# Performance work log

Measured on AMD Instinct MI355X. Metric: run time of the kernel, lower is better.

The kernel has to match this reference:

```python
import jax, jax.numpy as jnp
import numpy as np

N_T, D_MODEL, RANK, BATCH = 64, 1024, 8, 4096
THRESHOLD = 0.0  # jumprelu threshold (forward default)


def setup_inputs() -> dict:
    key = jax.random.key(0)
    k_x, k_v, k_u, k_e = jax.random.split(key, 4)
    scale = (1.0 / (D_MODEL * RANK)) ** 0.25
    x = jax.random.normal(k_x, (BATCH, D_MODEL), dtype=jnp.float32)
    V = jax.random.normal(k_v, (N_T, RANK, D_MODEL), dtype=jnp.float32) * scale
    U = jax.random.normal(k_u, (N_T, D_MODEL, RANK), dtype=jnp.float32) * scale
    encoder = jax.random.normal(k_e, (N_T, D_MODEL), dtype=jnp.float32)
    encoder = encoder / jnp.linalg.norm(encoder, axis=1, keepdims=True)
    bias = -jnp.ones((N_T,), dtype=jnp.float32)  # init_constant(bias, -1.0)
    return {"x": x, "V": V, "U": U, "encoder": encoder, "bias": bias}


def jumprelu(x, threshold=THRESHOLD):
    # forward: hard threshold x * 1[x > threshold]
    return x * (x > threshold).astype(x.dtype)


def reference(x, V, U, encoder, bias):
    # pre_acts: (batch, n)
    pre_acts = x @ encoder.T - bias
    gate = jumprelu(pre_acts)  # activation_fn='jumprelu', threshold=0.0
    # Vx: (n, batch, rank)
    Vx = jnp.einsum('nrd,bd->nbr', V, x)
    # UVx: (n, batch, d) -- the large intermediate a fused kernel would avoid
    UVx = jnp.einsum('ndr,nbr->nbd', U, Vx)
    # gated sum over transforms: (batch, d)
    output = jnp.einsum('nbd,bn->bd', UVx, gate)
    u_norms = jnp.linalg.norm(U.reshape(U.shape[0], -1), axis=1)
    v_norms = jnp.linalg.norm(V.reshape(V.shape[0], -1), axis=1)
    frobenius_norms = u_norms * v_norms / (D_MODEL * RANK) ** 0.5
    return output, gate, frobenius_norms
```

## Files before the change

kernel.cpp:

```cpp
#include <hip/hip_runtime.h>
#include <math.h>

#define BATCHN 4096
#define DMODEL 1024
#define NT 64
#define RANK 8
#define K2 512

typedef __attribute__((ext_vector_type(8))) short bf16x8;
typedef __attribute__((ext_vector_type(4))) float f32x4;

__device__ __forceinline__ void async16(void* lds, const void* g) {
    __builtin_amdgcn_global_load_lds(
        (const __attribute__((address_space(1))) void*)g,
        (__attribute__((address_space(3))) void*)lds, 16, 0, 0);
}

__device__ __forceinline__ short f2bf(float f) {
    unsigned u = __builtin_bit_cast(unsigned, f);
    u += 0x7fffu + ((u >> 16) & 1u);
    return (short)(u >> 16);
}

__global__ __launch_bounds__(256) void convert_kernel(
    const float* __restrict__ x, const float* __restrict__ enc,
    const float* __restrict__ V, const float* __restrict__ U,
    unsigned short* __restrict__ xb, unsigned short* __restrict__ Wb,
    unsigned short* __restrict__ Ub2)
{
    const int b = blockIdx.x, t = threadIdx.x;
    const float* src;
    unsigned short* dst;
    if (b < 2048) {
        const int e0 = b * 2048 + t * 8;
        src = x + e0; dst = xb + e0;
    } else if (b < 2336) {
        const int e0 = (b - 2048) * 2048 + t * 8;
        const int row = e0 >> 10, col = e0 & 1023;
        src = (row < 64) ? (enc + (size_t)row * 1024 + col)
                         : (V + (size_t)(row - 64) * 1024 + col);
        dst = Wb + e0;
    } else {
        const int e0 = (b - 2336) * 2048 + t * 8;
        const int d = e0 >> 9, j0 = e0 & 511;
        src = U + (size_t)(j0 >> 3) * (DMODEL * RANK) + (size_t)d * 8;
        dst = Ub2 + e0;
    }
    float4 v0 = *(const float4*)src;
    float4 v1 = *(const float4*)(src + 4);
    bf16x8 o;
    o[0] = f2bf(v0.x); o[1] = f2bf(v0.y); o[2] = f2bf(v0.z); o[3] = f2bf(v0.w);
    o[4] = f2bf(v1.x); o[5] = f2bf(v1.y); o[6] = f2bf(v1.z); o[7] = f2bf(v1.w);
    *(bf16x8*)dst = o;
}

__global__ __launch_bounds__(256) void gatevx_kernel(
    const unsigned short* __restrict__ A, const unsigned short* __restrict__ Bm,
    const float* __restrict__ bias,
    float* __restrict__ gate_out, unsigned short* __restrict__ vx_out)
{
    constexpr int BM = 128, BK = 64, BN = 64, TN = 2, KDIM = DMODEL;
    __shared__ unsigned short As[BM * BK];
    __shared__ unsigned short Bs[BN * BK];
    const int t = threadIdx.x;
    const int wave = t >> 6, lane = t & 63;
    const int bm = blockIdx.y, bn = blockIdx.x;
    const int wm = wave & 1, wn = wave >> 1;
    const int lrow = lane >> 3, lchunk = lane & 7;
    const int l15 = lane & 15, lq = lane >> 4;

    f32x4 acc[4][TN] = {};
    const size_t Abase = (size_t)bm * BM * KDIM;
    const size_t Bbase = (size_t)bn * BN * KDIM;

    for (int k0 = 0; k0 < KDIM; k0 += BK) {
        #pragma unroll
        for (int c = 0; c < 4; ++c) {
            const int row = (wave * 4 + c) * 8 + lrow;
            async16(&As[(wave * 4 + c) * 512],
                    A + Abase + (size_t)row * KDIM + k0 + ((lchunk ^ lrow) * 8));
        }
        #pragma unroll
        for (int c = 0; c < TN; ++c) {
            const int row = (wave * TN + c) * 8 + lrow;
            async16(&Bs[(wave * TN + c) * 512],
                    Bm + Bbase + (size_t)row * KDIM + k0 + ((lchunk ^ lrow) * 8));
        }
        __syncthreads();
        #pragma unroll
        for (int s = 0; s < 2; ++s) {
            bf16x8 af[4], bfr[TN];
            const int kc = s * 4 + lq;
            #pragma unroll
            for (int i = 0; i < 4; ++i) {
                const int m = wm * 64 + i * 16 + l15;
                af[i] = *(const bf16x8*)&As[m * BK + ((kc ^ (m & 7)) * 8)];
            }
            #pragma unroll
            for (int j = 0; j < TN; ++j) {
                const int n = wn * (TN * 16) + j * 16 + l15;
                bfr[j] = *(const bf16x8*)&Bs[n * BK + ((kc ^ (n & 7)) * 8)];
            }
            #pragma unroll
            for (int i = 0; i < 4; ++i)
                #pragma unroll
                for (int j = 0; j < TN; ++j)
                    acc[i][j] = __builtin_amdgcn_mfma_f32_16x16x32_bf16(
                        af[i], bfr[j], acc[i][j], 0, 0, 0);
        }
        __syncthreads();
    }

    #pragma unroll
    for (int i = 0; i < 4; ++i) {
        const int rowb = bm * BM + wm * 64 + i * 16 + lq * 4;
        #pragma unroll
        for (int j = 0; j < TN; ++j) {
            const int col = wn * (TN * 16) + j * 16 + l15;
            #pragma unroll
            for (int r = 0; r < 4; ++r) {
                const int row = rowb + r;
                const float v = acc[i][j][r];
                if (bn == 0) {
                    const float p = v - bias[col];
                    gate_out[(size_t)row * NT + col] = p > 0.f ? p : 0.f;
                } else {
                    vx_out[(size_t)row * K2 + (bn - 1) * 64 + col] = (unsigned short)f2bf(v);
                }
            }
        }
    }
}

__global__ __launch_bounds__(256) void out_kernel(
    const unsigned short* __restrict__ vx, const float* __restrict__ gate,
    const unsigned short* __restrict__ Bm, float* __restrict__ out)
{
    constexpr int BM = 128, BK = 64, BN = 128, TN = 4, KDIM = K2;
    __shared__ unsigned short As[BM * BK];
    __shared__ unsigned short Bs[BN * BK];
    const int t = threadIdx.x;
    const int wave = t >> 6, lane = t & 63;
    const int bm = blockIdx.y, bn = blockIdx.x;
    const int wm = wave & 1, wn = wave >> 1;
    const int lrow = lane >> 3, lchunk = lane & 7;
    const int l15 = lane & 15, lq = lane >> 4;

    f32x4 acc[4][TN] = {};
    const size_t Bbase = (size_t)bn * BN * KDIM;

    for (int k0 = 0; k0 < KDIM; k0 += BK) {
        #pragma unroll
        for (int c = 0; c < 4; ++c) {
            const int row = (wave * 4 + c) * 8 + lrow;
            const int grow = bm * BM + row;
            const int chunk = lchunk ^ lrow;
            bf16x8 v = *(const bf16x8*)(vx + (size_t)grow * K2 + k0 + chunk * 8);
            const float g = gate[(size_t)grow * NT + (k0 >> 3) + chunk];
            bf16x8 o;
            #pragma unroll
            for (int e = 0; e < 8; ++e) {
                const float f = __builtin_bit_cast(float,
                    ((unsigned)(unsigned short)v[e]) << 16);
                o[e] = (short)(__builtin_bit_cast(unsigned, f * g) >> 16);
            }
            *(bf16x8*)&As[(wave * 4 + c) * 512 + lane * 8] = o;
        }
        #pragma unroll
        for (int c = 0; c < TN; ++c) {
            const int row = (wave * TN + c) * 8 + lrow;
            async16(&Bs[(wave * TN + c) * 512],
                    Bm + Bbase + (size_t)row * KDIM + k0 + ((lchunk ^ lrow) * 8));
        }
        __syncthreads();
        #pragma unroll
        for (int s = 0; s < 2; ++s) {
            bf16x8 af[4], bfr[TN];
            const int kc = s * 4 + lq;
            #pragma unroll
            for (int i = 0; i < 4; ++i) {
                const int m = wm * 64 + i * 16 + l15;
                af[i] = *(const bf16x8*)&As[m * BK + ((kc ^ (m & 7)) * 8)];
            }
            #pragma unroll
            for (int j = 0; j < TN; ++j) {
                const int n = wn * (TN * 16) + j * 16 + l15;
                bfr[j] = *(const bf16x8*)&Bs[n * BK + ((kc ^ (n & 7)) * 8)];
            }
            #pragma unroll
            for (int i = 0; i < 4; ++i)
                #pragma unroll
                for (int j = 0; j < TN; ++j)
                    acc[i][j] = __builtin_amdgcn_mfma_f32_16x16x32_bf16(
                        af[i], bfr[j], acc[i][j], 0, 0, 0);
        }
        __syncthreads();
    }

    #pragma unroll
    for (int i = 0; i < 4; ++i) {
        const int rowb = bm * BM + wm * 64 + i * 16 + lq * 4;
        #pragma unroll
        for (int j = 0; j < TN; ++j) {
            const int col = bn * BN + wn * (TN * 16) + j * 16 + l15;
            #pragma unroll
            for (int r = 0; r < 4; ++r)
                out[(size_t)(rowb + r) * DMODEL + col] = acc[i][j][r];
        }
    }
}

__global__ __launch_bounds__(256) void norms_kernel(
    const float* __restrict__ U, const float* __restrict__ V, float* __restrict__ fro)
{
    const int n = blockIdx.x;
    const int t = threadIdx.x;
    float su = 0.f, sv = 0.f;
    for (int i = t; i < DMODEL * RANK; i += 256) {
        float u = U[(size_t)n * DMODEL * RANK + i];
        float v = V[(size_t)n * DMODEL * RANK + i];
        su += u * u;
        sv += v * v;
    }
    #pragma unroll
    for (int off = 32; off; off >>= 1) {
        su += __shfl_down(su, off);
        sv += __shfl_down(sv, off);
    }
    __shared__ float red[8];
    const int wave = t >> 6;
    if ((t & 63) == 0) { red[wave * 2] = su; red[wave * 2 + 1] = sv; }
    __syncthreads();
    if (t == 0) {
        float tu = 0.f, tv = 0.f;
        #pragma unroll
        for (int w = 0; w < 4; ++w) { tu += red[w * 2]; tv += red[w * 2 + 1]; }
        fro[n] = sqrtf(tu) * sqrtf(tv) / sqrtf((float)(DMODEL * RANK));
    }
}

extern "C" void kernel_launch(void* const* d_in, const int* in_sizes, int n_in,
                              void* d_out, int out_size, void* d_ws, size_t ws_size,
                              hipStream_t stream) {
    const float* x    = (const float*)d_in[0];
    const float* V    = (const float*)d_in[1];
    const float* U    = (const float*)d_in[2];
    const float* enc  = (const float*)d_in[3];
    const float* bias = (const float*)d_in[4];

    float* out  = (float*)d_out;
    float* gate = out + (size_t)BATCHN * DMODEL;
    float* fro  = gate + (size_t)BATCHN * NT;

    char* ws = (char*)d_ws;
    unsigned short* xb  = (unsigned short*)ws;
    unsigned short* Wb  = (unsigned short*)(ws + 8388608);
    unsigned short* Ub2 = (unsigned short*)(ws + 9568256);
    unsigned short* vx  = (unsigned short*)(ws + 10616832);

    convert_kernel<<<2592, 256, 0, stream>>>(x, enc, V, U, xb, Wb, Ub2);
    gatevx_kernel<<<dim3(9, 32), 256, 0, stream>>>(xb, Wb, bias, gate, vx);
    out_kernel<<<dim3(8, 32), 256, 0, stream>>>(vx, gate, Ub2, out);
    norms_kernel<<<64, 256, 0, stream>>>(U, V, fro);
}
```

Measured before the change: 126.7 us.

## Fuse Frobenius norms into convert/out kernels, shrink GEMM tiles, load U natively

```diff
diff --git a/kernel.cpp b/kernel.cpp
--- a/kernel.cpp
+++ b/kernel.cpp
@@ -26,25 +26,32 @@
     const float* __restrict__ x, const float* __restrict__ enc,
     const float* __restrict__ V, const float* __restrict__ U,
     unsigned short* __restrict__ xb, unsigned short* __restrict__ Wb,
-    unsigned short* __restrict__ Ub2)
+    unsigned short* __restrict__ Ub,
+    float* __restrict__ su_part, float* __restrict__ sv_part)
 {
     const int b = blockIdx.x, t = threadIdx.x;
     const float* src;
     unsigned short* dst;
+    float* psum = nullptr;
     if (b < 2048) {
         const int e0 = b * 2048 + t * 8;
         src = x + e0; dst = xb + e0;
     } else if (b < 2336) {
         const int e0 = (b - 2048) * 2048 + t * 8;
         const int row = e0 >> 10, col = e0 & 1023;
-        src = (row < 64) ? (enc + (size_t)row * 1024 + col)
-                         : (V + (size_t)(row - 64) * 1024 + col);
+        if (row < 64) {
+            src = enc + (size_t)row * 1024 + col;
+        } else {
+            src = V + (size_t)(row - 64) * 1024 + col;
+            const int vrow = (b - 2048) * 2 - 64;
+            psum = sv_part + (vrow >> 3) * 4 + ((vrow & 7) >> 1);
+        }
         dst = Wb + e0;
     } else {
-        const int e0 = (b - 2336) * 2048 + t * 8;
-        const int d = e0 >> 9, j0 = e0 & 511;
-        src = U + (size_t)(j0 >> 3) * (DMODEL * RANK) + (size_t)d * 8;
-        dst = Ub2 + e0;
+        const int bi = b - 2336;
+        const int e0 = bi * 2048 + t * 8;
+        src = U + e0; dst = Ub + e0;
+        psum = su_part + (bi >> 2) * 4 + (bi & 3);
     }
     float4 v0 = *(const float4*)src;
     float4 v1 = *(const float4*)(src + 4);
@@ -52,6 +59,17 @@
     o[0] = f2bf(v0.x); o[1] = f2bf(v0.y); o[2] = f2bf(v0.z); o[3] = f2bf(v0.w);
     o[4] = f2bf(v1.x); o[5] = f2bf(v1.y); o[6] = f2bf(v1.z); o[7] = f2bf(v1.w);
     *(bf16x8*)dst = o;
+
+    if (psum) {
+        float s = v0.x*v0.x + v0.y*v0.y + v0.z*v0.z + v0.w*v0.w
+                + v1.x*v1.x + v1.y*v1.y + v1.z*v1.z + v1.w*v1.w;
+        #pragma unroll
+        for (int off = 32; off; off >>= 1) s += __shfl_down(s, off);
+        __shared__ float red[4];
+        if ((t & 63) == 0) red[t >> 6] = s;
+        __syncthreads();
+        if (t == 0) *psum = red[0] + red[1] + red[2] + red[3];
+    }
 }
 
 __global__ __launch_bounds__(256) void gatevx_kernel(
@@ -59,9 +77,9 @@
     const float* __restrict__ bias,
     float* __restrict__ gate_out, unsigned short* __restrict__ vx_out)
 {
-    constexpr int BM = 128, BK = 64, BN = 64, TN = 2, KDIM = DMODEL;
-    __shared__ unsigned short As[BM * BK];
-    __shared__ unsigned short Bs[BN * BK];
+    constexpr int BK = 64, KDIM = DMODEL;
+    __shared__ unsigned short As[64 * BK];
+    __shared__ unsigned short Bs[64 * BK];
     const int t = threadIdx.x;
     const int wave = t >> 6, lane = t & 63;
     const int bm = blockIdx.y, bn = blockIdx.x;
@@ -69,42 +87,39 @@
     const int lrow = lane >> 3, lchunk = lane & 7;
     const int l15 = lane & 15, lq = lane >> 4;
 
-    f32x4 acc[4][TN] = {};
-    const size_t Abase = (size_t)bm * BM * KDIM;
-    const size_t Bbase = (size_t)bn * BN * KDIM;
+    f32x4 acc[2][2] = {};
+    const size_t Abase = (size_t)bm * 64 * KDIM;
+    const size_t Bbase = (size_t)bn * 64 * KDIM;
 
     for (int k0 = 0; k0 < KDIM; k0 += BK) {
         #pragma unroll
-        for (int c = 0; c < 4; ++c) {
-            const int row = (wave * 4 + c) * 8 + lrow;
-            async16(&As[(wave * 4 + c) * 512],
-                    A + Abase + (size_t)row * KDIM + k0 + ((lchunk ^ lrow) * 8));
-        }
-        #pragma unroll
-        for (int c = 0; c < TN; ++c) {
-            const int row = (wave * TN + c) * 8 + lrow;
-            async16(&Bs[(wave * TN + c) * 512],
-                    Bm + Bbase + (size_t)row * KDIM + k0 + ((lchunk ^ lrow) * 8));
+        for (int c = 0; c < 2; ++c) {
+            const int row = (wave * 2 + c) * 8 + lrow;
+            const int chunk = lchunk ^ lrow;
+            async16(&As[(wave * 2 + c) * 512],
+                    A + Abase + (size_t)row * KDIM + k0 + chunk * 8);
+            async16(&Bs[(wave * 2 + c) * 512],
+                    Bm + Bbase + (size_t)row * KDIM + k0 + chunk * 8);
         }
         __syncthreads();
         #pragma unroll
         for (int s = 0; s < 2; ++s) {
-            bf16x8 af[4], bfr[TN];
+            bf16x8 af[2], bfr[2];
             const int kc = s * 4 + lq;
             #pragma unroll
-            for (int i = 0; i < 4; ++i) {
-                const int m = wm * 64 + i * 16 + l15;
+            for (int i = 0; i < 2; ++i) {
+                const int m = wm * 32 + i * 16 + l15;
                 af[i] = *(const bf16x8*)&As[m * BK + ((kc ^ (m & 7)) * 8)];
             }
             #pragma unroll
-            for (int j = 0; j < TN; ++j) {
-                const int n = wn * (TN * 16) + j * 16 + l15;
+            for (int j = 0; j < 2; ++j) {
+                const int n = wn * 32 + j * 16 + l15;
                 bfr[j] = *(const bf16x8*)&Bs[n * BK + ((kc ^ (n & 7)) * 8)];
             }
             #pragma unroll
-            for (int i = 0; i < 4; ++i)
+            for (int i = 0; i < 2; ++i)
                 #pragma unroll
-                for (int j = 0; j < TN; ++j)
+                for (int j = 0; j < 2; ++j)
                     acc[i][j] = __builtin_amdgcn_mfma_f32_16x16x32_bf16(
                         af[i], bfr[j], acc[i][j], 0, 0, 0);
         }
@@ -112,11 +127,11 @@
     }
 
     #pragma unroll
-    for (int i = 0; i < 4; ++i) {
-        const int rowb = bm * BM + wm * 64 + i * 16 + lq * 4;
-        #pragma unroll
-        for (int j = 0; j < TN; ++j) {
-            const int col = wn * (TN * 16) + j * 16 + l15;
+    for (int i = 0; i < 2; ++i) {
+        const int rowb = bm * 64 + wm * 32 + i * 16 + lq * 4;
+        #pragma unroll
+        for (int j = 0; j < 2; ++j) {
+            const int col = wn * 32 + j * 16 + l15;
             #pragma unroll
             for (int r = 0; r < 4; ++r) {
                 const int row = rowb + r;
@@ -134,11 +149,13 @@
 
 __global__ __launch_bounds__(256) void out_kernel(
     const unsigned short* __restrict__ vx, const float* __restrict__ gate,
-    const unsigned short* __restrict__ Bm, float* __restrict__ out)
+    const unsigned short* __restrict__ Ub, float* __restrict__ out,
+    const float* __restrict__ su_part, const float* __restrict__ sv_part,
+    float* __restrict__ fro)
 {
-    constexpr int BM = 128, BK = 64, BN = 128, TN = 4, KDIM = K2;
-    __shared__ unsigned short As[BM * BK];
-    __shared__ unsigned short Bs[BN * BK];
+    constexpr int BK = 64, KDIM = K2;
+    __shared__ unsigned short As[64 * BK];
+    __shared__ unsigned short Bs[8 * 2 * 64 * 8];
     const int t = threadIdx.x;
     const int wave = t >> 6, lane = t & 63;
     const int bm = blockIdx.y, bn = blockIdx.x;
@@ -146,14 +163,13 @@
     const int lrow = lane >> 3, lchunk = lane & 7;
     const int l15 = lane & 15, lq = lane >> 4;
 
-    f32x4 acc[4][TN] = {};
-    const size_t Bbase = (size_t)bn * BN * KDIM;
+    f32x4 acc[2][4] = {};
 
     for (int k0 = 0; k0 < KDIM; k0 += BK) {
         #pragma unroll
-        for (int c = 0; c < 4; ++c) {
-            const int row = (wave * 4 + c) * 8 + lrow;
-            const int grow = bm * BM + row;
+        for (int c = 0; c < 2; ++c) {
+            const int row = (wave * 2 + c) * 8 + lrow;
+            const int grow = bm * 64 + row;
             const int chunk = lchunk ^ lrow;
             bf16x8 v = *(const bf16x8*)(vx + (size_t)grow * K2 + k0 + chunk * 8);
             const float g = gate[(size_t)grow * NT + (k0 >> 3) + chunk];
@@ -164,33 +180,36 @@
                     ((unsigned)(unsigned short)v[e]) << 16);
                 o[e] = (short)(__builtin_bit_cast(unsigned, f * g) >> 16);
             }
-            *(bf16x8*)&As[(wave * 4 + c) * 512 + lane * 8] = o;
-        }
-        #pragma unroll
-        for (int c = 0; c < TN; ++c) {
-            const int row = (wave * TN + c) * 8 + lrow;
-            async16(&Bs[(wave * TN + c) * 512],
-                    Bm + Bbase + (size_t)row * KDIM + k0 + ((lchunk ^ lrow) * 8));
+            *(bf16x8*)&As[(wave * 2 + c) * 512 + lane * 8] = o;
+        }
+        #pragma unroll
+        for (int c = 0; c < 4; ++c) {
+            const int n_local = wave * 2 + (c >> 1);
+            const int dblk = c & 1;
+            const int n_glob = (k0 >> 3) + n_local;
+            async16(&Bs[(n_local * 2 + dblk) * 512],
+                    Ub + (size_t)n_glob * (DMODEL * RANK)
+                       + (size_t)(bn * 128 + dblk * 64 + lane) * RANK);
         }
         __syncthreads();
         #pragma unroll
         for (int s = 0; s < 2; ++s) {
-            bf16x8 af[4], bfr[TN];
+            bf16x8 af[2], bfr[4];
             const int kc = s * 4 + lq;
             #pragma unroll
-            for (int i = 0; i < 4; ++i) {
-                const int m = wm * 64 + i * 16 + l15;
+            for (int i = 0; i < 2; ++i) {
+                const int m = wm * 32 + i * 16 + l15;
                 af[i] = *(const bf16x8*)&As[m * BK + ((kc ^ (m & 7)) * 8)];
             }
             #pragma unroll
-            for (int j = 0; j < TN; ++j) {
-                const int n = wn * (TN * 16) + j * 16 + l15;
-                bfr[j] = *(const bf16x8*)&Bs[n * BK + ((kc ^ (n & 7)) * 8)];
-            }
-            #pragma unroll
-            for (int i = 0; i < 4; ++i)
+            for (int j = 0; j < 4; ++j) {
+                const int cl = wn * 64 + j * 16 + l15;
+                bfr[j] = *(const bf16x8*)&Bs[((kc * 2 + (cl >> 6)) * 64 + (cl & 63)) * 8];
+            }
+            #pragma unroll
+            for (int i = 0; i < 2; ++i)
                 #pragma unroll
-                for (int j = 0; j < TN; ++j)
+                for (int j = 0; j < 4; ++j)
                     acc[i][j] = __builtin_amdgcn_mfma_f32_16x16x32_bf16(
                         af[i], bfr[j], acc[i][j], 0, 0, 0);
         }
@@ -198,44 +217,21 @@
     }
 
     #pragma unroll
-    for (int i = 0; i < 4; ++i) {
-        const int rowb = bm * BM + wm * 64 + i * 16 + lq * 4;
-        #pragma unroll
-        for (int j = 0; j < TN; ++j) {
-            const int col = bn * BN + wn * (TN * 16) + j * 16 + l15;
+    for (int i = 0; i < 2; ++i) {
+        const int rowb = bm * 64 + wm * 32 + i * 16 + lq * 4;
+        #pragma unroll
+        for (int j = 0; j < 4; ++j) {
+            const int col = bn * 128 + wn * 64 + j * 16 + l15;
             #pragma unroll
             for (int r = 0; r < 4; ++r)
                 out[(size_t)(rowb + r) * DMODEL + col] = acc[i][j][r];
         }
     }
-}
-
-__global__ __launch_bounds__(256) void norms_kernel(
-    const float* __restrict__ U, const float* __restrict__ V, float* __restrict__ fro)
-{
-    const int n = blockIdx.x;
-    const int t = threadIdx.x;
-    float su = 0.f, sv = 0.f;
-    for (int i = t; i < DMODEL * RANK; i += 256) {
-        float u = U[(size_t)n * DMODEL * RANK + i];
-        float v = V[(size_t)n * DMODEL * RANK + i];
-        su += u * u;
-        sv += v * v;
-    }
-    #pragma unroll
-    for (int off = 32; off; off >>= 1) {
-        su += __shfl_down(su, off);
-        sv += __shfl_down(sv, off);
-    }
-    __shared__ float red[8];
-    const int wave = t >> 6;
-    if ((t & 63) == 0) { red[wave * 2] = su; red[wave * 2 + 1] = sv; }
-    __syncthreads();
-    if (t == 0) {
-        float tu = 0.f, tv = 0.f;
-        #pragma unroll
-        for (int w = 0; w < 4; ++w) { tu += red[w * 2]; tv += red[w * 2 + 1]; }
-        fro[n] = sqrtf(tu) * sqrtf(tv) / sqrtf((float)(DMODEL * RANK));
+
+    if (bn == 0 && bm == 0 && t < NT) {
+        float su = su_part[t * 4] + su_part[t * 4 + 1] + su_part[t * 4 + 2] + su_part[t * 4 + 3];
+        float sv = sv_part[t * 4] + sv_part[t * 4 + 1] + sv_part[t * 4 + 2] + sv_part[t * 4 + 3];
+        fro[t] = sqrtf(su) * sqrtf(sv) / sqrtf((float)(DMODEL * RANK));
     }
 }
 
@@ -253,13 +249,14 @@
     float* fro  = gate + (size_t)BATCHN * NT;
 
     char* ws = (char*)d_ws;
-    unsigned short* xb  = (unsigned short*)ws;
-    unsigned short* Wb  = (unsigned short*)(ws + 8388608);
-    unsigned short* Ub2 = (unsigned short*)(ws + 9568256);
-    unsigned short* vx  = (unsigned short*)(ws + 10616832);
-
-    convert_kernel<<<2592, 256, 0, stream>>>(x, enc, V, U, xb, Wb, Ub2);
-    gatevx_kernel<<<dim3(9, 32), 256, 0, stream>>>(xb, Wb, bias, gate, vx);
-    out_kernel<<<dim3(8, 32), 256, 0, stream>>>(vx, gate, Ub2, out);
-    norms_kernel<<<64, 256, 0, stream>>>(U, V, fro);
-}
+    unsigned short* xb = (unsigned short*)ws;
+    unsigned short* Wb = (unsigned short*)(ws + 8388608);
+    unsigned short* Ub = (unsigned short*)(ws + 9568256);
+    unsigned short* vx = (unsigned short*)(ws + 10616832);
+    float* su_part     = (float*)(ws + 14811136);
+    float* sv_part     = (float*)(ws + 14812160);
+
+    convert_kernel<<<2592, 256, 0, stream>>>(x, enc, V, U, xb, Wb, Ub, su_part, sv_part);
+    gatevx_kernel<<<dim3(9, 64), 256, 0, stream>>>(xb, Wb, bias, gate, vx);
+    out_kernel<<<dim3(8, 64), 256, 0, stream>>>(vx, gate, Ub, out, su_part, sv_part, fro);
+}
```

New measurement: 105.8 us. 16.5% less time.
